# Kernel tuning notes

Hardware: AMD Instinct MI355X
Metric: run time of the kernel (lower is better)

## Reference

```python
import jax, jax.numpy as jnp
import numpy as np

EPS = 1e-7  # K.epsilon()

def squash(v, axis=-1):
    s2 = jnp.sum(jnp.square(v), axis=axis, keepdims=True)
    scale = s2 / (1.0 + s2) / jnp.sqrt(s2 + EPS)
    return scale * v

def setup_inputs() -> dict:
    key = jax.random.key(0)
    k1, k2 = jax.random.split(key)
    B, N, D_in = 128, 2048, 8
    J, P = 32, 16
    x = jax.random.normal(k1, (B, N, D_in), dtype=jnp.float32)
    W = jax.random.normal(k2, (J, N, P, D_in), dtype=jnp.float32) * 0.05
    return {"x": x, "W": W}

def reference(x, W):
    # x: [B, N, D_in]; W: [J, N, P, D_in]
    routings = 3
    J = W.shape[0]
    # inputs_hat: [B, J, N, P] -- u_hat_{j|n} = W_{jn} @ u_n
    inputs_hat = jnp.einsum('bni,jnpi->bjnp', x, W)
    B, _, N, _ = inputs_hat.shape
    b = jnp.zeros((B, J, N), dtype=inputs_hat.dtype)
    outputs = None
    for i in range(routings):
        c = jax.nn.softmax(b, axis=1)  # softmax over output capsules J
        s = jnp.einsum('bjn,bjnp->bjp', c, inputs_hat)
        outputs = squash(s)  # [B, J, P]
        if i < routings - 1:
            b = b + jnp.einsum('bjp,bjnp->bjn', outputs, inputs_hat)
    return outputs
```

## Files before the change

kernel.cpp:

```cpp
#include <hip/hip_runtime.h>
#include <math.h>

constexpr int Bb = 128;
constexpr int Nn = 2048;
constexpr int Dd = 8;
constexpr int Jj = 32;
constexpr int Pp = 16;

constexpr int BT = 2;
constexpr int WV = 8;
constexpr int BB = BT * WV;
constexpr int BN = 32;
constexpr int NBC = Bb / BB;
constexpr int NNC = Nn / BN;
constexpr int GRID = NBC * NNC;
constexpr int SZ = Bb * Jj * Pp;
constexpr size_t W16_ELEMS = (size_t)Jj * Nn * Pp * Dd;

typedef _Float16 half2v __attribute__((ext_vector_type(2)));
typedef _Float16 half8  __attribute__((ext_vector_type(8)));
typedef float    floatx4 __attribute__((ext_vector_type(4)));

#if __has_builtin(__builtin_amdgcn_fdot2)
__device__ inline float fdot2(half2v a, half2v b, float c) {
    return __builtin_amdgcn_fdot2(a, b, c, false);
}
#else
__device__ inline float fdot2(half2v a, half2v b, float c) {
    return (float)a.x * (float)b.x + (float)a.y * (float)b.y + c;
}
#endif

__device__ inline half2v bch2(unsigned u) { return __builtin_bit_cast(half2v, u); }
__device__ inline half8  bch8(uint4 u)    { return __builtin_bit_cast(half8, u); }
__device__ inline unsigned pkh2(float lo, float hi) {
    half2v h; h.x = (_Float16)lo; h.y = (_Float16)hi;
    return __builtin_bit_cast(unsigned, h);
}

template<int WT>
__global__ __launch_bounds__(512, 2)
void gemm0_k2(const float* __restrict__ x, const float* __restrict__ W,
              ushort* __restrict__ W16, float* __restrict__ S)
{
    __shared__ uint4 wl[2][256];
    __shared__ uint4 xl[2][512];

    const int tid  = threadIdx.x;
    const int wave = tid >> 6;
    const int lane = tid & 63;

    const int id  = blockIdx.x;
    const int xcd = id & 7;
    const int rem = id >> 3;
    const int jpc = rem & 7;
    const int nch = rem >> 3;
    const int nc  = xcd + 8 * nch;
    const int jp0 = jpc * 64;
    const int n0  = nc * 32;

    const int wns = (tid >> 6) & 3;
    const int wjpr = tid & 63;
    const int wjp = jp0 + wjpr, wj = wjp >> 4, wp = wjp & 15;
    const int xb = tid >> 2, xq = tid & 3;

    const float4* Wg = reinterpret_cast<const float4*>(W);
    const float4* Xg = reinterpret_cast<const float4*>(x);
    uint4* W16v = reinterpret_cast<uint4*>(W16);

    float4 wa, wb2, xa, xb2;
    auto load_t = [&](int ks) {
        const int n = n0 + ks * 4;
        if (tid < 256) {
            const size_t base = ((size_t)wj * 2048 + (n + wns)) * 32 + wp * 2;
            wa = Wg[base]; wb2 = Wg[base + 1];
        }
        const size_t xbase = ((size_t)xb * 2048 + n) * 2 + xq * 2;
        xa = Xg[xbase]; xb2 = Xg[xbase + 1];
    };
    auto store_t = [&](int buf, int ks) {
        if (tid < 256) {
            uint4 o;
            o.x = pkh2(wa.x, wa.y);   o.y = pkh2(wa.z, wa.w);
            o.z = pkh2(wb2.x, wb2.y); o.w = pkh2(wb2.z, wb2.w);
            wl[buf][tid] = o;
            if (WT)
                W16v[((size_t)wj * 2048 + (n0 + ks * 4 + wns)) * 16 + wp] = o;
        }
        uint4 o2;
        o2.x = pkh2(xa.x, xa.y);   o2.y = pkh2(xa.z, xa.w);
        o2.z = pkh2(xb2.x, xb2.y); o2.w = pkh2(xb2.z, xb2.w);
        xl[buf][xq * 128 + xb] = o2;
    };

    floatx4 acc[4];
    #pragma unroll
    for (int f = 0; f < 4; ++f)
        #pragma unroll
        for (int q = 0; q < 4; ++q) acc[f][q] = 0.f;

    load_t(0);
    store_t(0, 0);
    __syncthreads();

    const int kg = lane >> 4;
    const int ar = lane & 15;

    for (int ks = 0; ks < 8; ++ks) {
        if (ks < 7) load_t(ks + 1);
        const int buf = ks & 1;

        half8 bfrag = bch8(xl[buf][kg * 128 + wave * 16 + ar]);
        #pragma unroll
        for (int f = 0; f < 4; ++f) {
            half8 afrag = bch8(wl[buf][kg * 64 + f * 16 + ar]);
            acc[f] = __builtin_amdgcn_mfma_f32_16x16x32_f16(afrag, bfrag, acc[f], 0, 0, 0);
        }

        if (ks < 7) {
            store_t(buf ^ 1, ks + 1);
            __syncthreads();
        }
    }

    float* outp = S + (size_t)nc * SZ;
    const int bcol = wave * 16 + ar;
    #pragma unroll
    for (int f = 0; f < 4; ++f) {
        const size_t off = (size_t)bcol * 512 + jp0 + f * 16 + kg * 4;
        *reinterpret_cast<float4*>(outp + off) =
            make_float4(acc[f][0], acc[f][1], acc[f][2], acc[f][3]);
    }
}

template<int LOGITS, int ATOMIC, int W16F>
__global__ __launch_bounds__(512, 4)
void route_k(const float* __restrict__ x, const float* __restrict__ W,
             const ushort* __restrict__ W16,
             const float* __restrict__ OS, float* __restrict__ S)
{
    __shared__ uint4 wbuf[2][512];
    __shared__ uint4 xs[BB * BN];

    const int tid  = threadIdx.x;
    const int wave = tid >> 6;
    const int lane = tid & 63;

    const int id  = blockIdx.x;
    const int xcd = id & 7;
    const int bc  = (id >> 3) & 7;
    const int nch = id >> 6;
    const int nc  = xcd + 8 * nch;
    const int b0  = bc * BB;
    const int n0  = nc * BN;
    const int j   = lane >> 1;
    const int hp  = lane & 1;

    {
        const int b = tid >> 5, n = tid & 31;
        const float4* src = reinterpret_cast<const float4*>(
            x + ((size_t)(b0 + b) * Nn + n0 + n) * Dd);
        float4 a = src[0], c4 = src[1];
        uint4 o;
        o.x = pkh2(a.x, a.y);  o.y = pkh2(a.z, a.w);
        o.z = pkh2(c4.x, c4.y); o.w = pkh2(c4.z, c4.w);
        xs[b * BN + n] = o;
    }

    const float4* Wg = reinterpret_cast<const float4*>(W);
    const int sj = tid >> 4;
    const int sp = tid & 15;
    const int sl = sj * 2 + (sp >> 3);
    const int spp = sp & 7;
    const int wslot = spp * 64 + ((sl + spp) & 63);
    const int ispp = tid >> 6;
    const int isl  = ((tid & 63) - ispp) & 63;
    const int isj  = isl >> 1;
    const int isp  = ((isl & 1) << 3) | ispp;
    const uint4* W16v = reinterpret_cast<const uint4*>(W16);
    const size_t wbase16 = (size_t)isj * 32768 + isp;

    float4 sta, stb;
    uint4 st16;
    auto load_slice = [&](int n) {
        if (W16F) {
            st16 = W16v[wbase16 + (size_t)n * 16];
        } else {
            const size_t base = (size_t)n * 32 + sp * 2 + (size_t)sj * ((size_t)Nn * 32);
            sta = Wg[base];
            stb = Wg[base + 1];
        }
    };
    auto store_slice = [&](int buf) {
        if (W16F) {
            wbuf[buf][tid] = st16;
        } else {
            uint4 o;
            o.x = pkh2(sta.x, sta.y);  o.y = pkh2(sta.z, sta.w);
            o.z = pkh2(stb.x, stb.y);  o.w = pkh2(stb.z, stb.w);
            wbuf[buf][wslot] = o;
        }
    };

    float osum[BT][8];
    if (LOGITS) {
        #pragma unroll
        for (int bb = 0; bb < BT; ++bb) {
            const float4* op = reinterpret_cast<const float4*>(
                OS + ((size_t)(b0 + wave * BT + bb) * Jj + j) * Pp + hp * 8);
            float4 a = op[0], b4 = op[1];
            osum[bb][0] = a.x;  osum[bb][1] = a.y;  osum[bb][2] = a.z;  osum[bb][3] = a.w;
            osum[bb][4] = b4.x; osum[bb][5] = b4.y; osum[bb][6] = b4.z; osum[bb][7] = b4.w;
        }
    }

    float Sa[BT][8];
    #pragma unroll
    for (int bb = 0; bb < BT; ++bb)
        #pragma unroll
        for (int pp = 0; pp < 8; ++pp) Sa[bb][pp] = 0.f;

    load_slice(n0);
    store_slice(0);
    __syncthreads();

    const uint4* xw = xs + (size_t)(wave * BT) * BN;

    for (int nn = 0; nn < BN; ++nn) {
        if (nn + 1 < BN) load_slice(n0 + nn + 1);
        const int buf = nn & 1;

        half2v x01[BT], x23[BT], x45[BT], x67[BT];
        #pragma unroll
        for (int bb = 0; bb < BT; ++bb) {
            uint4 xr = xw[(size_t)bb * BN + nn];
            x01[bb] = bch2(xr.x); x23[bb] = bch2(xr.y);
            x45[bb] = bch2(xr.z); x67[bb] = bch2(xr.w);
        }

        float uh[BT][8];
        #pragma unroll
        for (int pp = 0; pp < 8; ++pp) {
            uint4 wv = wbuf[buf][pp * 64 + ((lane + pp) & 63)];
            half2v w01 = bch2(wv.x), w23 = bch2(wv.y);
            half2v w45 = bch2(wv.z), w67 = bch2(wv.w);
            #pragma unroll
            for (int bb = 0; bb < BT; ++bb) {
                float acc = fdot2(w01, x01[bb], 0.f);
                acc = fdot2(w23, x23[bb], acc);
                acc = fdot2(w45, x45[bb], acc);
                acc = fdot2(w67, x67[bb], acc);
                uh[bb][pp] = acc;
            }
        }

        if (!LOGITS) {
            #pragma unroll
            for (int bb = 0; bb < BT; ++bb)
                #pragma unroll
                for (int pp = 0; pp < 8; ++pp) Sa[bb][pp] += uh[bb][pp];
        } else {
            #pragma unroll
            for (int bb = 0; bb < BT; ++bb) {
                float lg = 0.f;
                #pragma unroll
                for (int pp = 0; pp < 8; ++pp)
                    lg = fmaf(osum[bb][pp], uh[bb][pp], lg);
                lg += __shfl_xor(lg, 1, 64);
                float e = __expf(lg);
                float se = e;
                #pragma unroll
                for (int mk = 2; mk <= 32; mk <<= 1)
                    se += __shfl_xor(se, mk, 64);
                float c = e * __builtin_amdgcn_rcpf(se);
                #pragma unroll
                for (int pp = 0; pp < 8; ++pp)
                    Sa[bb][pp] = fmaf(c, uh[bb][pp], Sa[bb][pp]);
            }
        }

        if (nn + 1 < BN) {
            store_slice((nn + 1) & 1);
            __syncthreads();
        }
    }

    #pragma unroll
    for (int bb = 0; bb < BT; ++bb) {
        const size_t off = ((size_t)(b0 + wave * BT + bb) * Jj + j) * Pp + hp * 8;
        if (ATOMIC) {
            float* spd = S + off;
            #pragma unroll
            for (int pp = 0; pp < 8; ++pp) atomicAdd(spd + pp, Sa[bb][pp]);
        } else {
            float4* dst = reinterpret_cast<float4*>(S + (size_t)nc * SZ + off);
            dst[0] = make_float4(Sa[bb][0], Sa[bb][1], Sa[bb][2], Sa[bb][3]);
            dst[1] = make_float4(Sa[bb][4], Sa[bb][5], Sa[bb][6], Sa[bb][7]);
        }
    }
}

__global__ void reduce_squash_k(const float* __restrict__ Sp, int nparts,
                                float scale, float* __restrict__ OS,
                                float* __restrict__ out, int mode)
{
    const int t = blockIdx.x * 64 + threadIdx.x;
    const float4* sp = reinterpret_cast<const float4*>(Sp);
    float4 a = make_float4(0.f, 0.f, 0.f, 0.f);
    #pragma unroll 8
    for (int s = 0; s < nparts; ++s) {
        float4 v = sp[(size_t)s * (SZ / 4) + t];
        a.x += v.x; a.y += v.y; a.z += v.z; a.w += v.w;
    }
    a.x *= scale; a.y *= scale; a.z *= scale; a.w *= scale;
    float s2 = a.x * a.x + a.y * a.y + a.z * a.z + a.w * a.w;
    s2 += __shfl_xor(s2, 1, 64);
    s2 += __shfl_xor(s2, 2, 64);
    const float g = s2 / ((1.f + s2) * sqrtf(s2 + 1e-7f));
    float4 v = make_float4(g * a.x, g * a.y, g * a.z, g * a.w);
    if (mode == 0) {
        reinterpret_cast<float4*>(OS)[t] = v;
    } else if (mode == 1) {
        float4 o = reinterpret_cast<float4*>(OS)[t];
        o.x += v.x; o.y += v.y; o.z += v.z; o.w += v.w;
        reinterpret_cast<float4*>(OS)[t] = o;
    } else {
        reinterpret_cast<float4*>(out)[t] = v;
    }
}

extern "C" void kernel_launch(void* const* d_in, const int* in_sizes, int n_in,
                              void* d_out, int out_size, void* d_ws, size_t ws_size,
                              hipStream_t stream)
{
    const float* x = (const float*)d_in[0];
    const float* W = (const float*)d_in[1];
    float* out = (float*)d_out;

    const size_t needSp = (size_t)(NNC + 1) * SZ * sizeof(float);
    const bool part  = ws_size >= needSp;
    const bool w16ok = ws_size >= needSp + W16_ELEMS * sizeof(ushort);
    dim3 rg(GRID), rb(512);
    dim3 sg(SZ / 4 / 64), sb(64);

    if (part) {
        float* Sp = (float*)d_ws;
        float* OS = Sp + (size_t)NNC * SZ;
        ushort* W16 = (ushort*)(OS + SZ);

        if (w16ok) {
            gemm0_k2<1><<<dim3(512), rb, 0, stream>>>(x, W, W16, Sp);
            reduce_squash_k<<<sg, sb, 0, stream>>>(Sp, NNC, 1.f / Jj, OS, out, 0);

            route_k<1, 0, 1><<<rg, rb, 0, stream>>>(x, W, W16, OS, Sp);
            reduce_squash_k<<<sg, sb, 0, stream>>>(Sp, NNC, 1.f, OS, out, 1);

            route_k<1, 0, 1><<<rg, rb, 0, stream>>>(x, W, W16, OS, Sp);
            reduce_squash_k<<<sg, sb, 0, stream>>>(Sp, NNC, 1.f, OS, out, 2);
        } else {
            gemm0_k2<0><<<dim3(512), rb, 0, stream>>>(x, W, nullptr, Sp);
            reduce_squash_k<<<sg, sb, 0, stream>>>(Sp, NNC, 1.f / Jj, OS, out, 0);

            route_k<1, 0, 0><<<rg, rb, 0, stream>>>(x, W, nullptr, OS, Sp);
            reduce_squash_k<<<sg, sb, 0, stream>>>(Sp, NNC, 1.f, OS, out, 1);

            route_k<1, 0, 0><<<rg, rb, 0, stream>>>(x, W, nullptr, OS, Sp);
            reduce_squash_k<<<sg, sb, 0, stream>>>(Sp, NNC, 1.f, OS, out, 2);
        }
    } else {
        float* S  = (float*)d_ws;
        float* OS = S + SZ;
        const size_t Sbytes = (size_t)SZ * sizeof(float);

        hipMemsetAsync(S, 0, Sbytes, stream);
        route_k<0, 1, 0><<<rg, rb, 0, stream>>>(x, W, nullptr, nullptr, S);
        reduce_squash_k<<<sg, sb, 0, stream>>>(S, 1, 1.f / Jj, OS, out, 0);

        hipMemsetAsync(S, 0, Sbytes, stream);
        route_k<1, 1, 0><<<rg, rb, 0, stream>>>(x, W, nullptr, OS, S);
        reduce_squash_k<<<sg, sb, 0, stream>>>(S, 1, 1.f, OS, out, 1);

        hipMemsetAsync(S, 0, Sbytes, stream);
        route_k<1, 1, 0><<<rg, rb, 0, stream>>>(x, W, nullptr, OS, S);
        reduce_squash_k<<<sg, sb, 0, stream>>>(S, 1, 1.f, OS, out, 2);
    }
}
```

Before: 204.3 us.

## Split fp16 weight conversion into its own kernel and add an MFMA first-iteration GEMM

Weight conversion to fp16 moves out of the first routing GEMM into a standalone streaming kernel. A new first-iteration kernel reads the prepared fp16 weights and uses 16x16x32 fp16 MFMA, staging the whole x tile in LDS once instead of double-buffering W and x. This removes conversion work and LDS staging from the GEMM, but adds a kernel launch and an extra full write and read of W16 in place of the previously fused conversion.

New measurement: 206.8 us. Within noise of the previous version (+1.2%).

```diff
diff --git a/kernel.cpp b/kernel.cpp
--- a/kernel.cpp
+++ b/kernel.cpp
@@ -36,6 +36,85 @@
 __device__ inline unsigned pkh2(float lo, float hi) {
     half2v h; h.x = (_Float16)lo; h.y = (_Float16)hi;
     return __builtin_bit_cast(unsigned, h);
+}
+
+__global__ __launch_bounds__(256)
+void w16cvt_k(const float* __restrict__ W, ushort* __restrict__ W16)
+{
+    const size_t g = (size_t)blockIdx.x * 256 + threadIdx.x;
+    const float4* Wg = reinterpret_cast<const float4*>(W);
+    float4 a = Wg[2 * g], b = Wg[2 * g + 1];
+    uint4 o;
+    o.x = pkh2(a.x, a.y); o.y = pkh2(a.z, a.w);
+    o.z = pkh2(b.x, b.y); o.w = pkh2(b.z, b.w);
+    reinterpret_cast<uint4*>(W16)[g] = o;
+}
+
+__global__ __launch_bounds__(512, 2)
+void gemm0_v3(const float* __restrict__ x, const ushort* __restrict__ W16,
+              float* __restrict__ S)
+{
+    __shared__ uint4 xl[32 * 128];
+
+    const int tid  = threadIdx.x;
+    const int wave = tid >> 6;
+    const int lane = tid & 63;
+
+    const int id  = blockIdx.x;
+    const int xcd = id & 7;
+    const int rem = id >> 3;
+    const int jpc = rem & 7;
+    const int nch = rem >> 3;
+    const int nc  = xcd + 8 * nch;
+    const int jp0 = jpc * 64;
+    const int n0  = nc * 32;
+
+    {
+        const int xb = tid >> 2, xq = tid & 3;
+        const float4* Xg = reinterpret_cast<const float4*>(x);
+        #pragma unroll
+        for (int r = 0; r < 8; ++r) {
+            const int nn = r * 4 + xq;
+            const size_t base = ((size_t)xb * 2048 + n0 + nn) * 2;
+            float4 a = Xg[base], b = Xg[base + 1];
+            uint4 o;
+            o.x = pkh2(a.x, a.y); o.y = pkh2(a.z, a.w);
+            o.z = pkh2(b.x, b.y); o.w = pkh2(b.z, b.w);
+            xl[nn * 128 + xb] = o;
+        }
+    }
+    __syncthreads();
+
+    const int ar = lane & 15;
+    const int kg = lane >> 4;
+
+    const uint4* W16v = reinterpret_cast<const uint4*>(W16);
+    const size_t abase = ((size_t)(jpc * 4) * 2048 + n0 + kg) * 16 + ar;
+
+    floatx4 acc[4];
+    #pragma unroll
+    for (int f = 0; f < 4; ++f)
+        #pragma unroll
+        for (int q = 0; q < 4; ++q) acc[f][q] = 0.f;
+
+    #pragma unroll
+    for (int ks = 0; ks < 8; ++ks) {
+        half8 bfrag = bch8(xl[(ks * 4 + kg) * 128 + wave * 16 + ar]);
+        #pragma unroll
+        for (int f = 0; f < 4; ++f) {
+            half8 afrag = bch8(W16v[abase + (size_t)f * 2048 * 16 + (size_t)ks * 4 * 16]);
+            acc[f] = __builtin_amdgcn_mfma_f32_16x16x32_f16(afrag, bfrag, acc[f], 0, 0, 0);
+        }
+    }
+
+    float* outp = S + (size_t)nc * SZ;
+    const int bcol = wave * 16 + ar;
+    #pragma unroll
+    for (int f = 0; f < 4; ++f) {
+        const size_t off = (size_t)bcol * 512 + jp0 + f * 16 + kg * 4;
+        *reinterpret_cast<float4*>(outp + off) =
+            make_float4(acc[f][0], acc[f][1], acc[f][2], acc[f][3]);
+    }
 }
 
 template<int WT>
@@ -349,7 +428,9 @@
         ushort* W16 = (ushort*)(OS + SZ);
 
         if (w16ok) {
-            gemm0_k2<1><<<dim3(512), rb, 0, stream>>>(x, W, W16, Sp);
+            const int cvtg = (int)(W16_ELEMS / 8 / 256);
+            w16cvt_k<<<dim3(cvtg), dim3(256), 0, stream>>>(W, W16);
+            gemm0_v3<<<dim3(512), rb, 0, stream>>>(x, W16, Sp);
             reduce_squash_k<<<sg, sb, 0, stream>>>(Sp, NNC, 1.f / Jj, OS, out, 0);
 
             route_k<1, 0, 1><<<rg, rb, 0, stream>>>(x, W, W16, OS, Sp);
```
